# Performance work log

Hardware: AMD Instinct MI355X
Metric: run time of the kernel (lower is better)

Reference implementation:

```python
import jax, jax.numpy as jnp
import numpy as np
import math

FEATURE_DIMS = [32, 64, 96, 128, 192, 256, 384, 512]
HIDDEN = 128
BATCH = 32768


def setup_inputs() -> dict:
    key = jax.random.key(0)
    keys = jax.random.split(key, 2 * len(FEATURE_DIMS) + len(FEATURE_DIMS) + 1)
    inp = {}
    # feature tensors (batch, dim_i)
    for i, d in enumerate(FEATURE_DIMS):
        inp[f"feat{i}"] = jax.random.normal(keys[i], (BATCH, d), dtype=jnp.float32)
    # per-feature key/value projection weights, torch nn.Linear layout (hidden, dim)
    n = len(FEATURE_DIMS)
    for i, d in enumerate(FEATURE_DIMS):
        bound = 1.0 / math.sqrt(d)
        inp[f"Wk{i}"] = jax.random.uniform(keys[n + i], (HIDDEN, d), dtype=jnp.float32, minval=-bound, maxval=bound)
        inp[f"Wv{i}"] = jax.random.uniform(keys[2 * n + i], (HIDDEN, d), dtype=jnp.float32, minval=-bound, maxval=bound)
    inp["query"] = jax.random.normal(keys[-1], (HIDDEN,), dtype=jnp.float32)
    return inp


def reference(feat0, feat1, feat2, feat3, feat4, feat5, feat6, feat7,
              Wk0, Wk1, Wk2, Wk3, Wk4, Wk5, Wk6, Wk7,
              Wv0, Wv1, Wv2, Wv3, Wv4, Wv5, Wv6, Wv7,
              query):
    feats = [feat0, feat1, feat2, feat3, feat4, feat5, feat6, feat7]
    Wks = [Wk0, Wk1, Wk2, Wk3, Wk4, Wk5, Wk6, Wk7]
    Wvs = [Wv0, Wv1, Wv2, Wv3, Wv4, Wv5, Wv6, Wv7]
    # per-feature projections: x @ W.T, torch Linear(bias=False) semantics
    K = jnp.stack([jnp.einsum('bd,hd->bh', f, W) for f, W in zip(feats, Wks)], axis=1)  # (B, F, H)
    V = jnp.stack([jnp.einsum('bd,hd->bh', f, W) for f, W in zip(feats, Wvs)], axis=1)  # (B, F, H)
    scores = jnp.einsum('bfh,h->bf', K, query) / math.sqrt(HIDDEN)  # (B, F)
    attn_weights = jax.nn.softmax(scores, axis=-1)
    combined = jnp.einsum('bf,bfh->bh', attn_weights, V)  # (B, H)
    # dropout is identity in eval mode
    return combined, attn_weights
```

## Files before the change

kernel.cpp:

```cpp
#include <hip/hip_runtime.h>
#include <hip/hip_bf16.h>

#define THREADS 256
#define HID     128
#define BATCH   32768
#define NFEAT   8
#define NCH     52

typedef __attribute__((ext_vector_type(4))) float f32x4;
typedef __attribute__((ext_vector_type(8))) short s16x8;

struct Ptrs {
    const float* feat[NFEAT];
    const float* wk[NFEAT];
    const float* wv[NFEAT];
    const float* q;
};

__device__ __forceinline__ unsigned short f2bf(float f) {
    union { __hip_bfloat16 h; unsigned short u; } c; c.h = __float2bfloat16(f); return c.u;
}

__device__ __forceinline__ s16x8 pack8(float4 x, float4 y) {
    s16x8 b;
    b[0] = (short)f2bf(x.x); b[1] = (short)f2bf(x.y);
    b[2] = (short)f2bf(x.z); b[3] = (short)f2bf(x.w);
    b[4] = (short)f2bf(y.x); b[5] = (short)f2bf(y.y);
    b[6] = (short)f2bf(y.z); b[7] = (short)f2bf(y.w);
    return b;
}

__device__ const int g_fdim[NFEAT] = {32, 64, 96, 128, 192, 256, 384, 512};
__device__ const int g_foff[NFEAT] = {0, 32, 96, 192, 320, 512, 768, 1152};
constexpr int c_fdim[NFEAT] = {32, 64, 96, 128, 192, 256, 384, 512};
constexpr int c_foff[NFEAT] = {0, 32, 96, 192, 320, 512, 768, 1152};

struct ChunkTab { int fi[NCH]; int ck[NCH]; };
constexpr ChunkTab make_tab() {
    ChunkTab t{};
    int c = 0;
    for (int f = 0; f < NFEAT; ++f)
        for (int k = 0; k < c_fdim[f]; k += 32) { t.fi[c] = f; t.ck[c] = k; ++c; }
    return t;
}
constexpr ChunkTab CT = make_tab();
static_assert(CT.fi[NCH - 1] == 7 && CT.ck[NCH - 1] == 480, "chunk table");

__global__ void prep_all(Ptrs p, unsigned short* WvB, float* qk) {
    int bid = blockIdx.x;
    if (bid < NFEAT * 8) {
        int fi    = bid >> 3;
        int slice = bid & 7;
        int D  = g_fdim[fi];
        int Dg = D >> 3;
        const float* Wv = p.wv[fi];
        unsigned short* out = WvB + 128 * g_foff[fi];
        int h0  = slice * 16;
        int cnt = 16 * Dg;
        for (int e = threadIdx.x; e < cnt; e += blockDim.x) {
            int h  = h0 + e / Dg;
            int kg = e - (e / Dg) * Dg;
            const float* src = Wv + h * D + kg * 8;
            float4 x = *reinterpret_cast<const float4*>(src);
            float4 y = *reinterpret_cast<const float4*>(src + 4);
            *reinterpret_cast<s16x8*>(out + (kg * 128 + h) * 8) = pack8(x, y);
        }
    } else {
        int i = bid - NFEAT * 8;
        int d = g_fdim[i];
        const float* Wk = p.wk[i];
        const float* q  = p.q;
        for (int c = threadIdx.x; c < d; c += blockDim.x) {
            float s = 0.f;
            #pragma unroll 8
            for (int h = 0; h < HID; ++h) s = fmaf(q[h], Wk[h * d + c], s);
            qk[g_foff[i] + c] = s * 0.08838834764831845f;
        }
    }
}


template<int FI, int CK0>
__device__ __forceinline__ void loadA1(const Ptrs& p, int rowg, int q4, float4 (&fa)[2]) {
    constexpr int D = c_fdim[FI];
    const float* b = p.feat[FI] + (size_t)rowg * D + CK0 + q4 * 8;
    fa[0] = *reinterpret_cast<const float4*>(b);
    fa[1] = *reinterpret_cast<const float4*>(b + 4);
}

template<int FI, int CK0>
__device__ __forceinline__ void loadB1(const unsigned short* WvB, int l15, int q4, s16x8 (&bb)[8]) {
    constexpr int FOFF = c_foff[FI];
    const unsigned short* Wb = WvB + 128 * FOFF + (size_t)(CK0 / 8 + q4) * 128 * 8 + l15 * 8;
    #pragma unroll
    for (int n = 0; n < 8; ++n)
        bb[n] = *reinterpret_cast<const s16x8*>(Wb + n * 16 * 8);
}

template<int C>
__device__ __forceinline__ void step(const Ptrs& p, const unsigned short* WvB, const float* qkS,
    int rowg, int l15, int q4,
    float4 (&fA)[3][2], s16x8 (&bf)[2][8],
    f32x4 (&P)[8], f32x4 (&O)[8], float& spart, float& Zacc, float (&wreg)[NFEAT])
{
    constexpr int FI   = CT.fi[C], CK0 = CT.ck[C];
    constexpr int D    = c_fdim[FI], FOFF = c_foff[FI];
    constexpr bool FIRST = (CK0 == 0), LAST = (CK0 + 32 == D);

    if constexpr (C + 1 < NCH) loadB1<CT.fi[C + 1], CT.ck[C + 1]>(WvB, l15, q4, bf[(C + 1) & 1]);
    if constexpr (C + 2 < NCH) loadA1<CT.fi[C + 2], CT.ck[C + 2]>(p, rowg, q4, fA[(C + 2) % 3]);
    __builtin_amdgcn_sched_barrier(0);

    if constexpr (FIRST) {
        spart = 0.f;
        #pragma unroll
        for (int n = 0; n < 8; ++n) P[n] = f32x4{0.f, 0.f, 0.f, 0.f};
    }

    float4 x = fA[C % 3][0], y = fA[C % 3][1];
    float4 q0 = *reinterpret_cast<const float4*>(qkS + FOFF + CK0 + q4 * 8);
    float4 q1 = *reinterpret_cast<const float4*>(qkS + FOFF + CK0 + q4 * 8 + 4);
    spart += x.x * q0.x + x.y * q0.y + x.z * q0.z + x.w * q0.w
           + y.x * q1.x + y.y * q1.y + y.z * q1.z + y.w * q1.w;
    s16x8 af = pack8(x, y);

    #pragma unroll
    for (int n = 0; n < 8; ++n)
        P[n] = __builtin_amdgcn_mfma_f32_16x16x32_bf16(af, bf[C & 1][n], P[n], 0, 0, 0);

    if constexpr (LAST) {
        float s = spart;
        s += __shfl_xor(s, 16, 64);
        s += __shfl_xor(s, 32, 64);
        float w = __expf(s);
        Zacc += w;
        wreg[FI] = w;
        #pragma unroll
        for (int rr = 0; rr < 4; ++rr) {
            float wr = __shfl(w, (q4 << 4) + q4 * 4 + rr, 64);
            #pragma unroll
            for (int n = 0; n < 8; ++n) O[n][rr] += wr * P[n][rr];
        }
    }
}

template<int C>
__device__ __forceinline__ void run_steps(const Ptrs& p, const unsigned short* WvB, const float* qkS,
    int rowg, int l15, int q4,
    float4 (&fA)[3][2], s16x8 (&bf)[2][8],
    f32x4 (&P)[8], f32x4 (&O)[8], float& spart, float& Zacc, float (&wreg)[NFEAT])
{
    step<C>(p, WvB, qkS, rowg, l15, q4, fA, bf, P, O, spart, Zacc, wreg);
    if constexpr (C + 1 < NCH)
        run_steps<C + 1>(p, WvB, qkS, rowg, l15, q4, fA, bf, P, O, spart, Zacc, wreg);
}

__global__ __launch_bounds__(THREADS, 2)
void attn_main(Ptrs p, const unsigned short* WvB, const float* qk,
               float* outC, float* outA) {
    __shared__ __align__(16) float qkS[1664];

    int tid  = threadIdx.x;
    int wave = tid >> 6;
    int lane = tid & 63;
    int l15  = lane & 15, q4 = lane >> 4;
    int rowbase = blockIdx.x * 64 + wave * 16;
    int rowg    = rowbase + l15;

    for (int g = tid; g < 1664; g += THREADS) qkS[g] = qk[g];
    __syncthreads();

    float4 fA[3][2];
    s16x8  bf[2][8];
    f32x4  P[8], O[8];
    float  spart = 0.f, Zacc = 0.f, wreg[NFEAT];
    #pragma unroll
    for (int n = 0; n < 8; ++n) O[n] = f32x4{0.f, 0.f, 0.f, 0.f};

    loadA1<0, 0>(p, rowg, q4, fA[0]);
    loadA1<1, 0>(p, rowg, q4, fA[1]);
    loadB1<0, 0>(WvB, l15, q4, bf[0]);

    run_steps<0>(p, WvB, qkS, rowg, l15, q4, fA, bf, P, O, spart, Zacc, wreg);

    float zi = 1.0f / Zacc;
    #pragma unroll
    for (int rr = 0; rr < 4; ++rr) {
        float zr = __shfl(zi, (q4 << 4) + q4 * 4 + rr, 64);
        int row = rowbase + q4 * 4 + rr;
        #pragma unroll
        for (int n = 0; n < 8; ++n)
            outC[(size_t)row * HID + n * 16 + l15] = O[n][rr] * zr;
    }
    if (q4 == 0) {
        float4 a0, a1;
        a0.x = wreg[0] * zi; a0.y = wreg[1] * zi; a0.z = wreg[2] * zi; a0.w = wreg[3] * zi;
        a1.x = wreg[4] * zi; a1.y = wreg[5] * zi; a1.z = wreg[6] * zi; a1.w = wreg[7] * zi;
        float* dst = outA + (size_t)rowg * NFEAT;
        *reinterpret_cast<float4*>(dst)     = a0;
        *reinterpret_cast<float4*>(dst + 4) = a1;
    }
}

extern "C" void kernel_launch(void* const* d_in, const int* in_sizes, int n_in,
                              void* d_out, int out_size, void* d_ws, size_t ws_size,
                              hipStream_t stream) {
    Ptrs p;
    for (int i = 0; i < NFEAT; ++i) {
        p.feat[i] = (const float*)d_in[i];
        p.wk[i]   = (const float*)d_in[NFEAT + 2 * i];
        p.wv[i]   = (const float*)d_in[NFEAT + 2 * i + 1];
    }
    p.q = (const float*)d_in[3 * NFEAT];

    unsigned short* WvB = (unsigned short*)d_ws;
    float* qk = (float*)((char*)d_ws + 128 * 1664 * 2);

    prep_all<<<NFEAT * 8 + NFEAT, 256, 0, stream>>>(p, WvB, qk);

    float* outC = (float*)d_out;
    float* outA = outC + (size_t)BATCH * HID;
    attn_main<<<BATCH / 64, THREADS, 0, stream>>>(p, WvB, qk, outC, outA);
}
```

Measured before the change: 287.5 us.

## Stage Wv chunks through LDS with async global_load_lds triple buffering

Each wave previously loaded its own full copy of the bf16 Wv chunk into registers from global memory. Now the four waves of a block load the chunk once, cooperatively and asynchronously, straight into a three-slot LDS ring using global_load_lds. Each wave then reads its B fragments from LDS, with explicit vmcnt waits and a block barrier every step. This cuts redundant global/L2 traffic for weights and register pressure, at the cost of 52 block-wide barriers and hand-tuned wait counts that must stay correct.

Result: faster. 279.8 us (-2.7%).

```diff
diff --git a/kernel.cpp b/kernel.cpp
--- a/kernel.cpp
+++ b/kernel.cpp
@@ -28,6 +28,12 @@
     b[4] = (short)f2bf(y.x); b[5] = (short)f2bf(y.y);
     b[6] = (short)f2bf(y.z); b[7] = (short)f2bf(y.w);
     return b;
+}
+
+__device__ __forceinline__ void glds16(const unsigned short* g, unsigned short* l) {
+    __builtin_amdgcn_global_load_lds(
+        (const __attribute__((address_space(1))) unsigned int*)g,
+        (__attribute__((address_space(3))) unsigned int*)l, 16, 0, 0);
 }
 
 __device__ const int g_fdim[NFEAT] = {32, 64, 96, 128, 192, 256, 384, 512};
@@ -88,27 +94,39 @@
     fa[1] = *reinterpret_cast<const float4*>(b + 4);
 }
 
-template<int FI, int CK0>
-__device__ __forceinline__ void loadB1(const unsigned short* WvB, int l15, int q4, s16x8 (&bb)[8]) {
-    constexpr int FOFF = c_foff[FI];
-    const unsigned short* Wb = WvB + 128 * FOFF + (size_t)(CK0 / 8 + q4) * 128 * 8 + l15 * 8;
-    #pragma unroll
-    for (int n = 0; n < 8; ++n)
-        bb[n] = *reinterpret_cast<const s16x8*>(Wb + n * 16 * 8);
-}
-
 template<int C>
-__device__ __forceinline__ void step(const Ptrs& p, const unsigned short* WvB, const float* qkS,
-    int rowg, int l15, int q4,
-    float4 (&fA)[3][2], s16x8 (&bf)[2][8],
-    f32x4 (&P)[8], f32x4 (&O)[8], float& spart, float& Zacc, float (&wreg)[NFEAT])
+__device__ __forceinline__ void issueB(const unsigned short* WvB, unsigned short* Bb,
+                                       int wave, int lane) {
+    constexpr int FI = CT.fi[C], CK0 = CT.ck[C];
+    const unsigned short* gs = WvB + (size_t)(128 * c_foff[FI] + 128 * CK0) + wave * 1024 + lane * 8;
+    unsigned short* ld = Bb + (C % 3) * 4096 + wave * 1024;
+    glds16(gs, ld);
+    glds16(gs + 512, ld + 512);
+}
+
+template<int C>
+__device__ __forceinline__ void step(const Ptrs& p, const unsigned short* WvB,
+    const float* qkS, unsigned short* Bb,
+    int rowg, int lane, int l15, int q4, int wave,
+    float4 (&fA)[3][2], f32x4 (&P)[8], f32x4 (&O)[8],
+    float& spart, float& Zacc, float (&wreg)[NFEAT])
 {
     constexpr int FI   = CT.fi[C], CK0 = CT.ck[C];
     constexpr int D    = c_fdim[FI], FOFF = c_foff[FI];
     constexpr bool FIRST = (CK0 == 0), LAST = (CK0 + 32 == D);
 
-    if constexpr (C + 1 < NCH) loadB1<CT.fi[C + 1], CT.ck[C + 1]>(WvB, l15, q4, bf[(C + 1) & 1]);
-    if constexpr (C + 2 < NCH) loadA1<CT.fi[C + 2], CT.ck[C + 2]>(p, rowg, q4, fA[(C + 2) % 3]);
+    const unsigned short* bb = Bb + (C % 3) * 4096 + (q4 * 128 + l15) * 8;
+    s16x8 bf[8];
+    #pragma unroll
+    for (int n = 0; n < 8; ++n)
+        bf[n] = *reinterpret_cast<const s16x8*>(bb + n * 128);
+    __builtin_amdgcn_sched_barrier(0);
+
+    if constexpr (C + 2 < NCH) {
+        issueB<C + 2>(WvB, Bb, wave, lane);
+        __builtin_amdgcn_sched_barrier(0);
+        loadA1<CT.fi[C + 2], CT.ck[C + 2]>(p, rowg, q4, fA[(C + 2) % 3]);
+    }
     __builtin_amdgcn_sched_barrier(0);
 
     if constexpr (FIRST) {
@@ -126,7 +144,7 @@
 
     #pragma unroll
     for (int n = 0; n < 8; ++n)
-        P[n] = __builtin_amdgcn_mfma_f32_16x16x32_bf16(af, bf[C & 1][n], P[n], 0, 0, 0);
+        P[n] = __builtin_amdgcn_mfma_f32_16x16x32_bf16(af, bf[n], P[n], 0, 0, 0);
 
     if constexpr (LAST) {
         float s = spart;
@@ -142,22 +160,33 @@
             for (int n = 0; n < 8; ++n) O[n][rr] += wr * P[n][rr];
         }
     }
+
+    __builtin_amdgcn_sched_barrier(0);
+    if constexpr (C + 1 < NCH) {
+        constexpr int NW = (C + 2 < NCH) ? 6 : 2;
+        asm volatile("s_waitcnt vmcnt(%0)" :: "i"(NW) : "memory");
+        __builtin_amdgcn_sched_barrier(0);
+        __builtin_amdgcn_s_barrier();
+        __builtin_amdgcn_sched_barrier(0);
+    }
 }
 
 template<int C>
-__device__ __forceinline__ void run_steps(const Ptrs& p, const unsigned short* WvB, const float* qkS,
-    int rowg, int l15, int q4,
-    float4 (&fA)[3][2], s16x8 (&bf)[2][8],
-    f32x4 (&P)[8], f32x4 (&O)[8], float& spart, float& Zacc, float (&wreg)[NFEAT])
+__device__ __forceinline__ void run_steps(const Ptrs& p, const unsigned short* WvB,
+    const float* qkS, unsigned short* Bb,
+    int rowg, int lane, int l15, int q4, int wave,
+    float4 (&fA)[3][2], f32x4 (&P)[8], f32x4 (&O)[8],
+    float& spart, float& Zacc, float (&wreg)[NFEAT])
 {
-    step<C>(p, WvB, qkS, rowg, l15, q4, fA, bf, P, O, spart, Zacc, wreg);
+    step<C>(p, WvB, qkS, Bb, rowg, lane, l15, q4, wave, fA, P, O, spart, Zacc, wreg);
     if constexpr (C + 1 < NCH)
-        run_steps<C + 1>(p, WvB, qkS, rowg, l15, q4, fA, bf, P, O, spart, Zacc, wreg);
+        run_steps<C + 1>(p, WvB, qkS, Bb, rowg, lane, l15, q4, wave, fA, P, O, spart, Zacc, wreg);
 }
 
 __global__ __launch_bounds__(THREADS, 2)
 void attn_main(Ptrs p, const unsigned short* WvB, const float* qk,
                float* outC, float* outA) {
+    __shared__ __align__(16) unsigned short Bb[3 * 4096];
     __shared__ __align__(16) float qkS[1664];
 
     int tid  = threadIdx.x;
@@ -167,21 +196,26 @@
     int rowbase = blockIdx.x * 64 + wave * 16;
     int rowg    = rowbase + l15;
 
-    for (int g = tid; g < 1664; g += THREADS) qkS[g] = qk[g];
-    __syncthreads();
-
     float4 fA[3][2];
-    s16x8  bf[2][8];
     f32x4  P[8], O[8];
     float  spart = 0.f, Zacc = 0.f, wreg[NFEAT];
     #pragma unroll
     for (int n = 0; n < 8; ++n) O[n] = f32x4{0.f, 0.f, 0.f, 0.f};
 
+    for (int g = tid; g < 1664; g += THREADS) qkS[g] = qk[g];
+    __builtin_amdgcn_sched_barrier(0);
+    issueB<0>(WvB, Bb, wave, lane);
+    issueB<1>(WvB, Bb, wave, lane);
+    __builtin_amdgcn_sched_barrier(0);
     loadA1<0, 0>(p, rowg, q4, fA[0]);
-    loadA1<1, 0>(p, rowg, q4, fA[1]);
-    loadB1<0, 0>(WvB, l15, q4, bf[0]);
-
-    run_steps<0>(p, WvB, qkS, rowg, l15, q4, fA, bf, P, O, spart, Zacc, wreg);
+    loadA1<CT.fi[1], CT.ck[1]>(p, rowg, q4, fA[1]);
+    __builtin_amdgcn_sched_barrier(0);
+    asm volatile("s_waitcnt vmcnt(4) lgkmcnt(0)" ::: "memory");
+    __builtin_amdgcn_sched_barrier(0);
+    __builtin_amdgcn_s_barrier();
+    __builtin_amdgcn_sched_barrier(0);
+
+    run_steps<0>(p, WvB, qkS, Bb, rowg, lane, l15, q4, wave, fA, P, O, spart, Zacc, wreg);
 
     float zi = 1.0f / Zacc;
     #pragma unroll
```
